# Kernel tuning notes

Measured on AMD Instinct MI355X. Metric: run time of the kernel, lower is better.

The kernel has to match this reference:

```python
import jax, jax.numpy as jnp
import numpy as np

B, S, H = 2, 2048, 1024
NH, HD = 16, 64  # num heads, head dim
EPS = 1e-12


def setup_inputs() -> dict:
    key = jax.random.key(0)
    ks = jax.random.split(key, 10)
    scale = 0.02
    return {
        "hidden_states": jax.random.normal(ks[0], (B, S, H), jnp.float32),
        "attention_mask": jnp.zeros((B, 1, 1, S), jnp.float32),
        "Wq": jax.random.normal(ks[1], (H, H), jnp.float32) * scale,
        "bq": jnp.zeros((H,), jnp.float32),
        "Wk": jax.random.normal(ks[2], (H, H), jnp.float32) * scale,
        "bk": jnp.zeros((H,), jnp.float32),
        "Wv": jax.random.normal(ks[3], (H, H), jnp.float32) * scale,
        "bv": jnp.zeros((H,), jnp.float32),
        "Wo": jax.random.normal(ks[4], (H, H), jnp.float32) * scale,
        "bo": jnp.zeros((H,), jnp.float32),
        "ln_gamma": jnp.ones((H,), jnp.float32),
        "ln_beta": jnp.zeros((H,), jnp.float32),
    }


def _split_heads(x):
    # [B,S,H] -> [B,NH,S,HD]
    b, s, _ = x.shape
    return x.reshape(b, s, NH, HD).transpose(0, 2, 1, 3)


def reference(hidden_states, attention_mask, Wq, bq, Wk, bk, Wv, bv, Wo, bo, ln_gamma, ln_beta):
    q = _split_heads(hidden_states @ Wq + bq)
    k = _split_heads(hidden_states @ Wk + bk)
    v = _split_heads(hidden_states @ Wv + bv)

    # unfused SDPA, as in source: matmul -> scale -> mask -> softmax -> matmul
    scores = jnp.einsum('bhqd,bhkd->bhqk', q, k) / jnp.sqrt(jnp.float32(HD))
    scores = scores + attention_mask
    probs = jax.nn.softmax(scores, axis=-1)  # dropout p=0 (eval)
    ctx = jnp.einsum('bhqk,bhkd->bhqd', probs, v)
    ctx = ctx.transpose(0, 2, 1, 3).reshape(hidden_states.shape)  # [B,S,H]

    # BaseBertSelfOutput: dense -> (dropout p=0) -> LayerNorm(residual)
    out = ctx @ Wo + bo
    res = out + hidden_states
    mu = jnp.mean(res, axis=-1, keepdims=True)
    var = jnp.mean(jnp.square(res - mu), axis=-1, keepdims=True)
    normed = (res - mu) * jax.lax.rsqrt(var + EPS)
    return normed * ln_gamma + ln_beta
```

## Files before the change

kernel.cpp:

```cpp
#include <hip/hip_runtime.h>
#include <hip/hip_bf16.h>

#define B_  2
#define S_  2048
#define H_  1024
#define NH_ 16
#define HD_ 64
#define EPSLN 1e-12f
#define LOG2E 1.4426950408889634f

typedef short bf16x8 __attribute__((ext_vector_type(8)));
typedef float f32x4  __attribute__((ext_vector_type(4)));
typedef float f32x16 __attribute__((ext_vector_type(16)));
typedef unsigned int u32x4 __attribute__((ext_vector_type(4)));

__device__ __forceinline__ float bf2f(ushort u) {
    union { unsigned int i; float f; } v; v.i = ((unsigned int)u) << 16; return v.f;
}
__device__ __forceinline__ ushort f2bf(float f) {
    union { float f; unsigned int i; } v; v.f = f;
    unsigned int r = v.i + 0x7FFFu + ((v.i >> 16) & 1u);
    return (ushort)(r >> 16);
}
__device__ __forceinline__ ushort f2bf_hw(float f) {
    __hip_bfloat16 h = __float2bfloat16(f);
    return *reinterpret_cast<ushort*>(&h);
}
__device__ __forceinline__ unsigned int pack_bf2(float a, float b) {
    return ((unsigned int)f2bf_hw(b) << 16) | (unsigned int)f2bf_hw(a);
}

__device__ __forceinline__ bf16x8 mk_pfrag(float a0, float a1, float a2, float a3,
                                           float a4, float a5, float a6, float a7, int hi) {
    unsigned int Lo0 = pack_bf2(a0, a1);
    unsigned int Lo1 = pack_bf2(a2, a3);
    unsigned int Hi0 = pack_bf2(a4, a5);
    unsigned int Hi1 = pack_bf2(a6, a7);
    unsigned int sLo0 = (unsigned int)__shfl_xor((int)Lo0, 32, 64);
    unsigned int sLo1 = (unsigned int)__shfl_xor((int)Lo1, 32, 64);
    unsigned int sHi0 = (unsigned int)__shfl_xor((int)Hi0, 32, 64);
    unsigned int sHi1 = (unsigned int)__shfl_xor((int)Hi1, 32, 64);
    u32x4 d;
    d.x = hi ? sHi0 : Lo0;
    d.y = hi ? sHi1 : Lo1;
    d.z = hi ? Hi0 : sLo0;
    d.w = hi ? Hi1 : sLo1;
    return __builtin_bit_cast(bf16x8, d);
}

__global__ __launch_bounds__(256) void cvt_f32_bf16(const float* __restrict__ in,
                                                    ushort* __restrict__ out, int n) {
    int i = (blockIdx.x * 256 + threadIdx.x) * 4;
    float4 v = *(const float4*)&in[i];
    ushort4 o = make_ushort4(f2bf(v.x), f2bf(v.y), f2bf(v.z), f2bf(v.w));
    *(ushort4*)&out[i] = o;
}

__global__ __launch_bounds__(256) void scale_mask(const float* __restrict__ in,
                                                  float* __restrict__ out) {
    int i = blockIdx.x * 256 + threadIdx.x;
    out[i] = in[i] * LOG2E;
}

__global__ __launch_bounds__(256) void transpose_cvt(
        const float* __restrict__ W0, const float* __restrict__ W1,
        const float* __restrict__ W2, const float* __restrict__ W3,
        ushort* __restrict__ T0, ushort* __restrict__ T1,
        ushort* __restrict__ T2, ushort* __restrict__ T3) {
    const int z = blockIdx.z;
    const float* in = (z == 0) ? W0 : (z == 1) ? W1 : (z == 2) ? W2 : W3;
    ushort* out     = (z == 0) ? T0 : (z == 1) ? T1 : (z == 2) ? T2 : T3;

    __shared__ float tile[64][65];
    const int bx = blockIdx.x * 64, by = blockIdx.y * 64;
    const int t = threadIdx.x;
    #pragma unroll
    for (int i = 0; i < 16; i++) {
        int idx = t + i * 256;
        int r = idx >> 6, c = idx & 63;
        tile[r][c] = in[(by + r) * 1024 + bx + c];
    }
    __syncthreads();
    #pragma unroll
    for (int i = 0; i < 16; i++) {
        int idx = t + i * 256;
        int r = idx >> 6, c = idx & 63;
        out[(bx + r) * 1024 + by + c] = f2bf(tile[c][r]);
    }
}

__global__ __launch_bounds__(256) void v_transpose(const ushort* __restrict__ Vb,
                                                   ushort* __restrict__ VtG) {
    __shared__ ushort tile[64][72];
    const int s0 = blockIdx.x * 64;
    const int head = blockIdx.y;
    const ushort* src = Vb + (size_t)head * S_ * HD_;
    ushort* dst       = VtG + (size_t)head * S_ * HD_;
    const int t = threadIdx.x, lane = t & 63, w = t >> 6;

    uint4 a = *(const uint4*)&src[(s0 + lane) * HD_ + w * 16];
    uint4 b = *(const uint4*)&src[(s0 + lane) * HD_ + w * 16 + 8];
    const ushort* pa = (const ushort*)&a;
    #pragma unroll
    for (int i = 0; i < 8; i++) tile[w * 16 + i][lane] = pa[i];
    const ushort* pb = (const ushort*)&b;
    #pragma unroll
    for (int i = 0; i < 8; i++) tile[w * 16 + 8 + i][lane] = pb[i];
    __syncthreads();

    const int d = t >> 2, sc = (t & 3) * 16;
    uint4 o1 = *(const uint4*)&tile[d][sc];
    uint4 o2 = *(const uint4*)&tile[d][sc + 8];
    *(uint4*)&dst[d * S_ + s0 + sc]     = o1;
    *(uint4*)&dst[d * S_ + s0 + sc + 8] = o2;
}

__global__ __launch_bounds__(256) void qkv_gemm(
        const ushort* __restrict__ X,
        const ushort* __restrict__ Wqt, const ushort* __restrict__ Wkt, const ushort* __restrict__ Wvt,
        const float* __restrict__ bq,  const float* __restrict__ bk,  const float* __restrict__ bv,
        ushort* __restrict__ Qo, ushort* __restrict__ Ko, ushort* __restrict__ Vo) {
    const int which = blockIdx.z;
    const ushort* Wt  = (which == 0) ? Wqt : (which == 1) ? Wkt : Wvt;
    const float* bias = (which == 0) ? bq  : (which == 1) ? bk  : bv;
    ushort* Out       = (which == 0) ? Qo  : (which == 1) ? Ko  : Vo;

    __shared__ ushort As[128][72];
    __shared__ ushort Bs[128][72];
    const int m0 = blockIdx.x * 128, n0 = blockIdx.y * 128;
    const int t = threadIdx.x;
    const int lane = t & 63, w = t >> 6;
    const int wr = (w >> 1) * 64, wc = (w & 1) * 64;
    const int l15 = lane & 15, l4 = lane >> 4;

    f32x4 acc[4][4] = {};
    const int sr = t >> 3, sc = (t & 7) * 8;

    for (int k0 = 0; k0 < H_; k0 += 64) {
        __syncthreads();
        #pragma unroll
        for (int p = 0; p < 4; p++) {
            uint4 av  = *(const uint4*)&X [(m0 + p * 32 + sr) * H_ + k0 + sc];
            uint4 bv2 = *(const uint4*)&Wt[(n0 + p * 32 + sr) * H_ + k0 + sc];
            *(uint4*)&As[p * 32 + sr][sc] = av;
            *(uint4*)&Bs[p * 32 + sr][sc] = bv2;
        }
        __syncthreads();
        #pragma unroll
        for (int ks = 0; ks < 2; ks++) {
            bf16x8 af[4], bfr[4];
            #pragma unroll
            for (int i = 0; i < 4; i++) af[i]  = *(const bf16x8*)&As[wr + i * 16 + l15][ks * 32 + l4 * 8];
            #pragma unroll
            for (int i = 0; i < 4; i++) bfr[i] = *(const bf16x8*)&Bs[wc + i * 16 + l15][ks * 32 + l4 * 8];
            #pragma unroll
            for (int mi = 0; mi < 4; mi++)
                #pragma unroll
                for (int ni = 0; ni < 4; ni++)
                    acc[mi][ni] = __builtin_amdgcn_mfma_f32_16x16x32_bf16(af[mi], bfr[ni], acc[mi][ni], 0, 0, 0);
        }
    }

    #pragma unroll
    for (int ni = 0; ni < 4; ni++) {
        int n = n0 + wc + ni * 16 + l15;
        float bvf = bias[n];
        int h = n >> 6, d = n & 63;
        #pragma unroll
        for (int mi = 0; mi < 4; mi++) {
            int mrow = m0 + wr + mi * 16 + l4 * 4;
            #pragma unroll
            for (int j = 0; j < 4; j++) {
                int m = mrow + j;
                int b = m >> 11, s = m & 2047;
                Out[((b * NH_ + h) * S_ + s) * HD_ + d] = f2bf(acc[mi][ni][j] + bvf);
            }
        }
    }
}

__global__ __launch_bounds__(128) void flash_attn(
        const ushort* __restrict__ Q, const ushort* __restrict__ K, const ushort* __restrict__ VtG,
        const float* __restrict__ maskL2, ushort* __restrict__ ctx) {
    __shared__ __align__(16) ushort Ks[64][72];
    __shared__ __align__(16) ushort Vt[64][72];

    const int wgid = blockIdx.x;
    const int vid  = (wgid & 7) * 128 + (wgid >> 3);
    const int qt   = vid & 31;
    const int hb   = vid >> 5;
    const int h    = hb & (NH_ - 1), b = hb >> 4;

    const int t = threadIdx.x, lane = t & 63, w = t >> 6;
    const int l31 = lane & 31, hi = lane >> 5;
    const size_t head_off = (size_t)hb * S_ * HD_;
    const ushort* Qh = Q + head_off;
    const ushort* Kh = K + head_off;
    const ushort* Vh = VtG + head_off;

    const int q0w  = qt * 64 + w * 32;
    const int qrow = q0w + l31;
    bf16x8 qf[4];
    #pragma unroll
    for (int kc = 0; kc < 4; kc++)
        qf[kc] = *(const bf16x8*)&Qh[qrow * 64 + kc * 16 + hi * 8];

    f32x16 acc0 = {}, acc1 = {};
    float mrun = -1e30f, lrun = 0.f;

    const float ksc = 0.125f * LOG2E;

    for (int kv0 = 0; kv0 < S_; kv0 += 64) {
        __syncthreads();
        #pragma unroll
        for (int it = 0; it < 4; it++) {
            int ci = it * 128 + t;
            int row = ci >> 3, ce = (ci & 7) * 8;
            *(uint4*)&Ks[row][ce] = *(const uint4*)&Kh[(kv0 + row) * 64 + ce];
            *(uint4*)&Vt[row][ce] = *(const uint4*)&Vh[row * S_ + kv0 + ce];
        }
        __syncthreads();

        f32x16 s0 = {}, s1 = {};
        #pragma unroll
        for (int kc = 0; kc < 4; kc++) {
            bf16x8 kf0 = *(const bf16x8*)&Ks[l31][kc * 16 + hi * 8];
            bf16x8 kf1 = *(const bf16x8*)&Ks[32 + l31][kc * 16 + hi * 8];
            s0 = __builtin_amdgcn_mfma_f32_32x32x16_bf16(kf0, qf[kc], s0, 0, 0, 0);
            s1 = __builtin_amdgcn_mfma_f32_32x32x16_bf16(kf1, qf[kc], s1, 0, 0, 0);
        }

        float tmax = -1e30f;
        #pragma unroll
        for (int g = 0; g < 4; g++) {
            float4 mk0 = *(const float4*)&maskL2[b * S_ + kv0 + g * 8 + hi * 4];
            float4 mk1 = *(const float4*)&maskL2[b * S_ + kv0 + 32 + g * 8 + hi * 4];
            #pragma unroll
            for (int j = 0; j < 4; j++) {
                int r = g * 4 + j;
                s0[r] = fmaf(s0[r], ksc, (&mk0.x)[j]);
                s1[r] = fmaf(s1[r], ksc, (&mk1.x)[j]);
                tmax = fmaxf(tmax, fmaxf(s0[r], s1[r]));
            }
        }
        tmax = fmaxf(tmax, __shfl_xor(tmax, 32, 64));

        if (!__all(tmax <= mrun + 8.0f)) {
            float mnew  = fmaxf(mrun, tmax);
            float scale = exp2f(mrun - mnew);
            mrun = mnew;
            lrun *= scale;
            #pragma unroll
            for (int r = 0; r < 16; r++) { acc0[r] *= scale; acc1[r] *= scale; }
        }

        float tsum = 0.f;
        #pragma unroll
        for (int r = 0; r < 16; r++) {
            s0[r] = exp2f(s0[r] - mrun);
            s1[r] = exp2f(s1[r] - mrun);
            tsum += s0[r] + s1[r];
        }
        tsum += __shfl_xor(tsum, 32, 64);
        lrun += tsum;

        bf16x8 pf0 = mk_pfrag(s0[0], s0[1], s0[2],  s0[3],  s0[4],  s0[5],  s0[6],  s0[7],  hi);
        bf16x8 pf1 = mk_pfrag(s0[8], s0[9], s0[10], s0[11], s0[12], s0[13], s0[14], s0[15], hi);
        bf16x8 pf2 = mk_pfrag(s1[0], s1[1], s1[2],  s1[3],  s1[4],  s1[5],  s1[6],  s1[7],  hi);
        bf16x8 pf3 = mk_pfrag(s1[8], s1[9], s1[10], s1[11], s1[12], s1[13], s1[14], s1[15], hi);

        {
            bf16x8 vf0, vf1;
            vf0 = *(const bf16x8*)&Vt[l31][0 * 16 + hi * 8];
            vf1 = *(const bf16x8*)&Vt[32 + l31][0 * 16 + hi * 8];
            acc0 = __builtin_amdgcn_mfma_f32_32x32x16_bf16(vf0, pf0, acc0, 0, 0, 0);
            acc1 = __builtin_amdgcn_mfma_f32_32x32x16_bf16(vf1, pf0, acc1, 0, 0, 0);
            vf0 = *(const bf16x8*)&Vt[l31][1 * 16 + hi * 8];
            vf1 = *(const bf16x8*)&Vt[32 + l31][1 * 16 + hi * 8];
            acc0 = __builtin_amdgcn_mfma_f32_32x32x16_bf16(vf0, pf1, acc0, 0, 0, 0);
            acc1 = __builtin_amdgcn_mfma_f32_32x32x16_bf16(vf1, pf1, acc1, 0, 0, 0);
            vf0 = *(const bf16x8*)&Vt[l31][2 * 16 + hi * 8];
            vf1 = *(const bf16x8*)&Vt[32 + l31][2 * 16 + hi * 8];
            acc0 = __builtin_amdgcn_mfma_f32_32x32x16_bf16(vf0, pf2, acc0, 0, 0, 0);
            acc1 = __builtin_amdgcn_mfma_f32_32x32x16_bf16(vf1, pf2, acc1, 0, 0, 0);
            vf0 = *(const bf16x8*)&Vt[l31][3 * 16 + hi * 8];
            vf1 = *(const bf16x8*)&Vt[32 + l31][3 * 16 + hi * 8];
            acc0 = __builtin_amdgcn_mfma_f32_32x32x16_bf16(vf0, pf3, acc0, 0, 0, 0);
            acc1 = __builtin_amdgcn_mfma_f32_32x32x16_bf16(vf1, pf3, acc1, 0, 0, 0);
        }
    }

    const float inv = 1.0f / lrun;
    const size_t rowbase = ((size_t)b * S_ + q0w + l31) * H_ + h * 64;
    #pragma unroll
    for (int g = 0; g < 4; g++) {
        ushort4 o0, o1;
        o0.x = f2bf(acc0[g * 4 + 0] * inv); o0.y = f2bf(acc0[g * 4 + 1] * inv);
        o0.z = f2bf(acc0[g * 4 + 2] * inv); o0.w = f2bf(acc0[g * 4 + 3] * inv);
        o1.x = f2bf(acc1[g * 4 + 0] * inv); o1.y = f2bf(acc1[g * 4 + 1] * inv);
        o1.z = f2bf(acc1[g * 4 + 2] * inv); o1.w = f2bf(acc1[g * 4 + 3] * inv);
        *(ushort4*)&ctx[rowbase + g * 8 + hi * 4]      = o0;
        *(ushort4*)&ctx[rowbase + 32 + g * 8 + hi * 4] = o1;
    }
}

__global__ __launch_bounds__(256) void out_proj(
        const ushort* __restrict__ Ctx, const ushort* __restrict__ Wot,
        const float* __restrict__ bo,  const float* __restrict__ Hs,
        float* __restrict__ Tmp) {
    __shared__ ushort As[128][72];
    __shared__ ushort Bs[128][72];
    const int m0 = blockIdx.x * 128, n0 = blockIdx.y * 128;
    const int t = threadIdx.x;
    const int lane = t & 63, w = t >> 6;
    const int wr = (w >> 1) * 64, wc = (w & 1) * 64;
    const int l15 = lane & 15, l4 = lane >> 4;

    f32x4 acc[4][4] = {};
    const int sr = t >> 3, sc = (t & 7) * 8;

    for (int k0 = 0; k0 < H_; k0 += 64) {
        __syncthreads();
        #pragma unroll
        for (int p = 0; p < 4; p++) {
            uint4 av  = *(const uint4*)&Ctx[(m0 + p * 32 + sr) * H_ + k0 + sc];
            uint4 bv2 = *(const uint4*)&Wot[(n0 + p * 32 + sr) * H_ + k0 + sc];
            *(uint4*)&As[p * 32 + sr][sc] = av;
            *(uint4*)&Bs[p * 32 + sr][sc] = bv2;
        }
        __syncthreads();
        #pragma unroll
        for (int ks = 0; ks < 2; ks++) {
            bf16x8 af[4], bfr[4];
            #pragma unroll
            for (int i = 0; i < 4; i++) af[i]  = *(const bf16x8*)&As[wr + i * 16 + l15][ks * 32 + l4 * 8];
            #pragma unroll
            for (int i = 0; i < 4; i++) bfr[i] = *(const bf16x8*)&Bs[wc + i * 16 + l15][ks * 32 + l4 * 8];
            #pragma unroll
            for (int mi = 0; mi < 4; mi++)
                #pragma unroll
                for (int ni = 0; ni < 4; ni++)
                    acc[mi][ni] = __builtin_amdgcn_mfma_f32_16x16x32_bf16(af[mi], bfr[ni], acc[mi][ni], 0, 0, 0);
        }
    }

    #pragma unroll
    for (int ni = 0; ni < 4; ni++) {
        int n = n0 + wc + ni * 16 + l15;
        float bvf = bo[n];
        #pragma unroll
        for (int mi = 0; mi < 4; mi++) {
            int mrow = m0 + wr + mi * 16 + l4 * 4;
            #pragma unroll
            for (int j = 0; j < 4; j++) {
                int m = mrow + j;
                Tmp[(size_t)m * H_ + n] = acc[mi][ni][j] + bvf + Hs[(size_t)m * H_ + n];
            }
        }
    }
}

__global__ __launch_bounds__(256) void ln_kernel(
        const float* __restrict__ Tmp, const float* __restrict__ gamma,
        const float* __restrict__ beta, float* __restrict__ Out) {
    const int row = blockIdx.x;
    const float* x = Tmp + (size_t)row * H_;
    const int t = threadIdx.x, w = t >> 6, lane = t & 63;

    float4 v = *(const float4*)&x[t * 4];
    float s = v.x + v.y + v.z + v.w;
    #pragma unroll
    for (int m = 1; m < 64; m <<= 1) s += __shfl_xor(s, m, 64);
    __shared__ float red[4], red2[4];
    if (lane == 0) red[w] = s;
    __syncthreads();
    float mu = (red[0] + red[1] + red[2] + red[3]) * (1.0f / H_);

    float d0 = v.x - mu, d1 = v.y - mu, d2 = v.z - mu, d3 = v.w - mu;
    float sq = d0 * d0 + d1 * d1 + d2 * d2 + d3 * d3;
    #pragma unroll
    for (int m = 1; m < 64; m <<= 1) sq += __shfl_xor(sq, m, 64);
    if (lane == 0) red2[w] = sq;
    __syncthreads();
    float var = (red2[0] + red2[1] + red2[2] + red2[3]) * (1.0f / H_);
    float rstd = rsqrtf(var + EPSLN);

    float dd[4] = {d0, d1, d2, d3};
    float4 o;
    o.x = dd[0] * rstd * gamma[t * 4 + 0] + beta[t * 4 + 0];
    o.y = dd[1] * rstd * gamma[t * 4 + 1] + beta[t * 4 + 1];
    o.z = dd[2] * rstd * gamma[t * 4 + 2] + beta[t * 4 + 2];
    o.w = dd[3] * rstd * gamma[t * 4 + 3] + beta[t * 4 + 3];
    *(float4*)&Out[(size_t)row * H_ + t * 4] = o;
}

extern "C" void kernel_launch(void* const* d_in, const int* in_sizes, int n_in,
                              void* d_out, int out_size, void* d_ws, size_t ws_size,
                              hipStream_t stream) {
    const float* hs    = (const float*)d_in[0];
    const float* mask  = (const float*)d_in[1];
    const float* Wq    = (const float*)d_in[2];
    const float* bq    = (const float*)d_in[3];
    const float* Wk    = (const float*)d_in[4];
    const float* bk    = (const float*)d_in[5];
    const float* Wv    = (const float*)d_in[6];
    const float* bv    = (const float*)d_in[7];
    const float* Wo    = (const float*)d_in[8];
    const float* bo    = (const float*)d_in[9];
    const float* gamma = (const float*)d_in[10];
    const float* beta  = (const float*)d_in[11];

    char* ws = (char*)d_ws;
    const size_t WSZ = (size_t)H_ * H_;
    const size_t TSZ = (size_t)B_ * S_ * H_;
    ushort* Wqt = (ushort*)ws;
    ushort* Wkt = Wqt + WSZ;
    ushort* Wvt = Wkt + WSZ;
    ushort* Wot = Wvt + WSZ;
    ushort* Xb  = Wot + WSZ;
    ushort* Qb  = Xb + TSZ;
    ushort* Kb  = Qb + TSZ;
    ushort* Vb  = Kb + TSZ;
    ushort* Ctx = Vb + TSZ;
    float*  Tmp = (float*)(Ctx + TSZ);
    ushort* VtG = (ushort*)Tmp;
    float* MaskL2 = (float*)Xb;

    cvt_f32_bf16<<<TSZ / (256 * 4), 256, 0, stream>>>(hs, Xb, (int)TSZ);
    transpose_cvt<<<dim3(16, 16, 4), 256, 0, stream>>>(Wq, Wk, Wv, Wo, Wqt, Wkt, Wvt, Wot);

    qkv_gemm<<<dim3(32, 8, 3), 256, 0, stream>>>(Xb, Wqt, Wkt, Wvt, bq, bk, bv, Qb, Kb, Vb);
    scale_mask<<<(B_ * S_) / 256, 256, 0, stream>>>(mask, MaskL2);
    v_transpose<<<dim3(S_ / 64, B_ * NH_), 256, 0, stream>>>(Vb, VtG);
    flash_attn<<<dim3(1024), 128, 0, stream>>>(Qb, Kb, VtG, MaskL2, Ctx);
    out_proj<<<dim3(32, 8), 256, 0, stream>>>(Ctx, Wot, bo, hs, Tmp);
    ln_kernel<<<B_ * S_, 256, 0, stream>>>(Tmp, gamma, beta, (float*)d_out);
}
```

Baseline: 169.7 us.

## Double-buffer K/V tiles with async global-to-LDS loads and XOR swizzle

```diff
diff --git a/kernel.cpp b/kernel.cpp
--- a/kernel.cpp
+++ b/kernel.cpp
@@ -28,6 +28,11 @@
 }
 __device__ __forceinline__ unsigned int pack_bf2(float a, float b) {
     return ((unsigned int)f2bf_hw(b) << 16) | (unsigned int)f2bf_hw(a);
+}
+
+__device__ __forceinline__ void gll16(const ushort* g, ushort* l) {
+    __builtin_amdgcn_global_load_lds((const __attribute__((address_space(1))) void*)g,
+                                     (__attribute__((address_space(3))) void*)l, 16, 0, 0);
 }
 
 __device__ __forceinline__ bf16x8 mk_pfrag(float a0, float a1, float a2, float a3,
@@ -182,8 +187,8 @@
 __global__ __launch_bounds__(128) void flash_attn(
         const ushort* __restrict__ Q, const ushort* __restrict__ K, const ushort* __restrict__ VtG,
         const float* __restrict__ maskL2, ushort* __restrict__ ctx) {
-    __shared__ __align__(16) ushort Ks[64][72];
-    __shared__ __align__(16) ushort Vt[64][72];
+    __shared__ __align__(16) ushort KsB[2][4096];
+    __shared__ __align__(16) ushort VtB[2][4096];
 
     const int wgid = blockIdx.x;
     const int vid  = (wgid & 7) * 128 + (wgid >> 3);
@@ -207,25 +212,40 @@
 
     f32x16 acc0 = {}, acc1 = {};
     float mrun = -1e30f, lrun = 0.f;
-
     const float ksc = 0.125f * LOG2E;
-
+    const int xm = (l31 & 7) << 3;
+
+    #pragma unroll
+    for (int it = 0; it < 4; it++) {
+        int ci = it * 128 + t;
+        int row = ci >> 3;
+        int ce = ((ci & 7) * 8) ^ ((row & 7) << 3);
+        gll16(&Kh[row * 64 + ce],  &KsB[0][it * 1024 + w * 512]);
+        gll16(&Vh[row * S_ + ce],  &VtB[0][it * 1024 + w * 512]);
+    }
+
+    int cur = 0;
     for (int kv0 = 0; kv0 < S_; kv0 += 64) {
         __syncthreads();
-        #pragma unroll
-        for (int it = 0; it < 4; it++) {
-            int ci = it * 128 + t;
-            int row = ci >> 3, ce = (ci & 7) * 8;
-            *(uint4*)&Ks[row][ce] = *(const uint4*)&Kh[(kv0 + row) * 64 + ce];
-            *(uint4*)&Vt[row][ce] = *(const uint4*)&Vh[row * S_ + kv0 + ce];
-        }
-        __syncthreads();
+        if (kv0 + 64 < S_) {
+            #pragma unroll
+            for (int it = 0; it < 4; it++) {
+                int ci = it * 128 + t;
+                int row = ci >> 3;
+                int ce = ((ci & 7) * 8) ^ ((row & 7) << 3);
+                gll16(&Kh[(kv0 + 64 + row) * 64 + ce], &KsB[cur ^ 1][it * 1024 + w * 512]);
+                gll16(&Vh[row * S_ + kv0 + 64 + ce],   &VtB[cur ^ 1][it * 1024 + w * 512]);
+            }
+        }
+        const ushort* KsL = KsB[cur];
+        const ushort* VtL = VtB[cur];
 
         f32x16 s0 = {}, s1 = {};
         #pragma unroll
         for (int kc = 0; kc < 4; kc++) {
-            bf16x8 kf0 = *(const bf16x8*)&Ks[l31][kc * 16 + hi * 8];
-            bf16x8 kf1 = *(const bf16x8*)&Ks[32 + l31][kc * 16 + hi * 8];
+            int ec = kc * 16 + hi * 8;
+            bf16x8 kf0 = *(const bf16x8*)&KsL[l31 * 64 + (ec ^ xm)];
+            bf16x8 kf1 = *(const bf16x8*)&KsL[(32 + l31) * 64 + (ec ^ xm)];
             s0 = __builtin_amdgcn_mfma_f32_32x32x16_bf16(kf0, qf[kc], s0, 0, 0, 0);
             s1 = __builtin_amdgcn_mfma_f32_32x32x16_bf16(kf1, qf[kc], s1, 0, 0, 0);
         }
@@ -271,23 +291,24 @@
 
         {
             bf16x8 vf0, vf1;
-            vf0 = *(const bf16x8*)&Vt[l31][0 * 16 + hi * 8];
-            vf1 = *(const bf16x8*)&Vt[32 + l31][0 * 16 + hi * 8];
+            vf0 = *(const bf16x8*)&VtL[l31 * 64 + ((0 * 16 + hi * 8) ^ xm)];
+            vf1 = *(const bf16x8*)&VtL[(32 + l31) * 64 + ((0 * 16 + hi * 8) ^ xm)];
             acc0 = __builtin_amdgcn_mfma_f32_32x32x16_bf16(vf0, pf0, acc0, 0, 0, 0);
             acc1 = __builtin_amdgcn_mfma_f32_32x32x16_bf16(vf1, pf0, acc1, 0, 0, 0);
-            vf0 = *(const bf16x8*)&Vt[l31][1 * 16 + hi * 8];
-            vf1 = *(const bf16x8*)&Vt[32 + l31][1 * 16 + hi * 8];
+            vf0 = *(const bf16x8*)&VtL[l31 * 64 + ((1 * 16 + hi * 8) ^ xm)];
+            vf1 = *(const bf16x8*)&VtL[(32 + l31) * 64 + ((1 * 16 + hi * 8) ^ xm)];
             acc0 = __builtin_amdgcn_mfma_f32_32x32x16_bf16(vf0, pf1, acc0, 0, 0, 0);
             acc1 = __builtin_amdgcn_mfma_f32_32x32x16_bf16(vf1, pf1, acc1, 0, 0, 0);
-            vf0 = *(const bf16x8*)&Vt[l31][2 * 16 + hi * 8];
-            vf1 = *(const bf16x8*)&Vt[32 + l31][2 * 16 + hi * 8];
+            vf0 = *(const bf16x8*)&VtL[l31 * 64 + ((2 * 16 + hi * 8) ^ xm)];
+            vf1 = *(const bf16x8*)&VtL[(32 + l31) * 64 + ((2 * 16 + hi * 8) ^ xm)];
             acc0 = __builtin_amdgcn_mfma_f32_32x32x16_bf16(vf0, pf2, acc0, 0, 0, 0);
             acc1 = __builtin_amdgcn_mfma_f32_32x32x16_bf16(vf1, pf2, acc1, 0, 0, 0);
-            vf0 = *(const bf16x8*)&Vt[l31][3 * 16 + hi * 8];
-            vf1 = *(const bf16x8*)&Vt[32 + l31][3 * 16 + hi * 8];
+            vf0 = *(const bf16x8*)&VtL[l31 * 64 + ((3 * 16 + hi * 8) ^ xm)];
+            vf1 = *(const bf16x8*)&VtL[(32 + l31) * 64 + ((3 * 16 + hi * 8) ^ xm)];
             acc0 = __builtin_amdgcn_mfma_f32_32x32x16_bf16(vf0, pf3, acc0, 0, 0, 0);
             acc1 = __builtin_amdgcn_mfma_f32_32x32x16_bf16(vf1, pf3, acc1, 0, 0, 0);
         }
+        cur ^= 1;
     }
 
     const float inv = 1.0f / lrun;
```

After: 175.5 us. +3.4%, slower.

## Split attention KV range in two and merge partials in a combine kernel

Applied to the files above, without the earlier changes.

```diff
diff --git a/kernel.cpp b/kernel.cpp
--- a/kernel.cpp
+++ b/kernel.cpp
@@ -181,15 +181,17 @@
 
 __global__ __launch_bounds__(128) void flash_attn(
         const ushort* __restrict__ Q, const ushort* __restrict__ K, const ushort* __restrict__ VtG,
-        const float* __restrict__ maskL2, ushort* __restrict__ ctx) {
+        const float* __restrict__ maskL2, ushort* __restrict__ Part, float2* __restrict__ ML) {
     __shared__ __align__(16) ushort Ks[64][72];
     __shared__ __align__(16) ushort Vt[64][72];
 
     const int wgid = blockIdx.x;
-    const int vid  = (wgid & 7) * 128 + (wgid >> 3);
-    const int qt   = vid & 31;
-    const int hb   = vid >> 5;
-    const int h    = hb & (NH_ - 1), b = hb >> 4;
+    const int vid  = (wgid & 7) * 256 + (wgid >> 3);
+    const int split = vid & 1;
+    const int qt    = (vid >> 1) & 31;
+    const int hb    = vid >> 6;
+    const int b     = hb >> 4;
+    const int kbase = split << 10;
 
     const int t = threadIdx.x, lane = t & 63, w = t >> 6;
     const int l31 = lane & 31, hi = lane >> 5;
@@ -207,10 +209,9 @@
 
     f32x16 acc0 = {}, acc1 = {};
     float mrun = -1e30f, lrun = 0.f;
-
     const float ksc = 0.125f * LOG2E;
 
-    for (int kv0 = 0; kv0 < S_; kv0 += 64) {
+    for (int kv0 = kbase; kv0 < kbase + 1024; kv0 += 64) {
         __syncthreads();
         #pragma unroll
         for (int it = 0; it < 4; it++) {
@@ -290,18 +291,48 @@
         }
     }
 
-    const float inv = 1.0f / lrun;
+    ushort* Pp = Part + (size_t)split * (B_ * S_ * H_);
+    const int h = hb & (NH_ - 1);
     const size_t rowbase = ((size_t)b * S_ + q0w + l31) * H_ + h * 64;
     #pragma unroll
     for (int g = 0; g < 4; g++) {
         ushort4 o0, o1;
-        o0.x = f2bf(acc0[g * 4 + 0] * inv); o0.y = f2bf(acc0[g * 4 + 1] * inv);
-        o0.z = f2bf(acc0[g * 4 + 2] * inv); o0.w = f2bf(acc0[g * 4 + 3] * inv);
-        o1.x = f2bf(acc1[g * 4 + 0] * inv); o1.y = f2bf(acc1[g * 4 + 1] * inv);
-        o1.z = f2bf(acc1[g * 4 + 2] * inv); o1.w = f2bf(acc1[g * 4 + 3] * inv);
-        *(ushort4*)&ctx[rowbase + g * 8 + hi * 4]      = o0;
-        *(ushort4*)&ctx[rowbase + 32 + g * 8 + hi * 4] = o1;
-    }
+        o0.x = f2bf(acc0[g * 4 + 0]); o0.y = f2bf(acc0[g * 4 + 1]);
+        o0.z = f2bf(acc0[g * 4 + 2]); o0.w = f2bf(acc0[g * 4 + 3]);
+        o1.x = f2bf(acc1[g * 4 + 0]); o1.y = f2bf(acc1[g * 4 + 1]);
+        o1.z = f2bf(acc1[g * 4 + 2]); o1.w = f2bf(acc1[g * 4 + 3]);
+        *(ushort4*)&Pp[rowbase + g * 8 + hi * 4]      = o0;
+        *(ushort4*)&Pp[rowbase + 32 + g * 8 + hi * 4] = o1;
+    }
+    if (hi == 0)
+        ML[(size_t)split * (B_ * NH_ * S_) + (size_t)hb * S_ + q0w + l31] = make_float2(mrun, lrun);
+}
+
+__global__ __launch_bounds__(256) void combine_kv(
+        const ushort* __restrict__ P0, const ushort* __restrict__ P1,
+        const float2* __restrict__ ML0, const float2* __restrict__ ML1,
+        ushort* __restrict__ ctx) {
+    const int row = blockIdx.x;
+    const int t = threadIdx.x;
+    const int b = row >> 11, s = row & 2047;
+    const int col = t * 4;
+    const int h = col >> 6;
+    const int hb = b * NH_ + h;
+
+    float2 a = ML0[(size_t)hb * S_ + s];
+    float2 c = ML1[(size_t)hb * S_ + s];
+    float M  = fmaxf(a.x, c.x);
+    float e0 = exp2f(a.x - M), e1 = exp2f(c.x - M);
+    float inv = 1.0f / (a.y * e0 + c.y * e1);
+
+    ushort4 p0 = *(const ushort4*)&P0[(size_t)row * H_ + col];
+    ushort4 p1 = *(const ushort4*)&P1[(size_t)row * H_ + col];
+    ushort4 o;
+    o.x = f2bf((bf2f(p0.x) * e0 + bf2f(p1.x) * e1) * inv);
+    o.y = f2bf((bf2f(p0.y) * e0 + bf2f(p1.y) * e1) * inv);
+    o.z = f2bf((bf2f(p0.z) * e0 + bf2f(p1.z) * e1) * inv);
+    o.w = f2bf((bf2f(p0.w) * e0 + bf2f(p1.w) * e1) * inv);
+    *(ushort4*)&ctx[(size_t)row * H_ + col] = o;
 }
 
 __global__ __launch_bounds__(256) void out_proj(
@@ -423,8 +454,10 @@
     ushort* Vb  = Kb + TSZ;
     ushort* Ctx = Vb + TSZ;
     float*  Tmp = (float*)(Ctx + TSZ);
-    ushort* VtG = (ushort*)Tmp;
-    float* MaskL2 = (float*)Xb;
+    float*  MaskL2 = (float*)Wqt;
+    float2* ML     = (float2*)Wkt;
+    ushort* VtG    = Xb;
+    ushort* Part   = (ushort*)Tmp;
 
     cvt_f32_bf16<<<TSZ / (256 * 4), 256, 0, stream>>>(hs, Xb, (int)TSZ);
     transpose_cvt<<<dim3(16, 16, 4), 256, 0, stream>>>(Wq, Wk, Wv, Wo, Wqt, Wkt, Wvt, Wot);
@@ -432,7 +465,9 @@
     qkv_gemm<<<dim3(32, 8, 3), 256, 0, stream>>>(Xb, Wqt, Wkt, Wvt, bq, bk, bv, Qb, Kb, Vb);
     scale_mask<<<(B_ * S_) / 256, 256, 0, stream>>>(mask, MaskL2);
     v_transpose<<<dim3(S_ / 64, B_ * NH_), 256, 0, stream>>>(Vb, VtG);
-    flash_attn<<<dim3(1024), 128, 0, stream>>>(Qb, Kb, VtG, MaskL2, Ctx);
+    flash_attn<<<dim3(2048), 128, 0, stream>>>(Qb, Kb, VtG, MaskL2, Part, ML);
+    combine_kv<<<dim3(B_ * S_), 256, 0, stream>>>(Part, Part + TSZ,
+                                                  ML, ML + (size_t)B_ * NH_ * S_, Ctx);
     out_proj<<<dim3(32, 8), 256, 0, stream>>>(Ctx, Wot, bo, hs, Tmp);
     ln_kernel<<<B_ * S_, 256, 0, stream>>>(Tmp, gamma, beta, (float*)d_out);
 }
```

Result: slower. 200.3 us (+18.1%).

## Use direct global-to-LDS loads in GEMMs and widen flash-attention workgroups

Applied to the files above, without the earlier changes.

```diff
diff --git a/kernel.cpp b/kernel.cpp
--- a/kernel.cpp
+++ b/kernel.cpp
@@ -28,6 +28,11 @@
 }
 __device__ __forceinline__ unsigned int pack_bf2(float a, float b) {
     return ((unsigned int)f2bf_hw(b) << 16) | (unsigned int)f2bf_hw(a);
+}
+
+__device__ __forceinline__ void gll16(const ushort* g, ushort* l) {
+    __builtin_amdgcn_global_load_lds((const __attribute__((address_space(1))) void*)g,
+                                     (__attribute__((address_space(3))) void*)l, 16, 0, 0);
 }
 
 __device__ __forceinline__ bf16x8 mk_pfrag(float a0, float a1, float a2, float a3,
@@ -125,8 +130,8 @@
     const float* bias = (which == 0) ? bq  : (which == 1) ? bk  : bv;
     ushort* Out       = (which == 0) ? Qo  : (which == 1) ? Ko  : Vo;
 
-    __shared__ ushort As[128][72];
-    __shared__ ushort Bs[128][72];
+    __shared__ __align__(16) ushort As[128 * 64];
+    __shared__ __align__(16) ushort Bs[128 * 64];
     const int m0 = blockIdx.x * 128, n0 = blockIdx.y * 128;
     const int t = threadIdx.x;
     const int lane = t & 63, w = t >> 6;
@@ -134,31 +139,30 @@
     const int l15 = lane & 15, l4 = lane >> 4;
 
     f32x4 acc[4][4] = {};
-    const int sr = t >> 3, sc = (t & 7) * 8;
 
     for (int k0 = 0; k0 < H_; k0 += 64) {
-        __syncthreads();
-        #pragma unroll
-        for (int p = 0; p < 4; p++) {
-            uint4 av  = *(const uint4*)&X [(m0 + p * 32 + sr) * H_ + k0 + sc];
-            uint4 bv2 = *(const uint4*)&Wt[(n0 + p * 32 + sr) * H_ + k0 + sc];
-            *(uint4*)&As[p * 32 + sr][sc] = av;
-            *(uint4*)&Bs[p * 32 + sr][sc] = bv2;
+        #pragma unroll
+        for (int it = 0; it < 4; it++) {
+            int ci = it * 256 + t;
+            int row = ci >> 3, col = (ci & 7) * 8;
+            gll16(&X [(m0 + row) * H_ + k0 + col], &As[ci * 8]);
+            gll16(&Wt[(n0 + row) * H_ + k0 + col], &Bs[ci * 8]);
         }
         __syncthreads();
         #pragma unroll
         for (int ks = 0; ks < 2; ks++) {
             bf16x8 af[4], bfr[4];
             #pragma unroll
-            for (int i = 0; i < 4; i++) af[i]  = *(const bf16x8*)&As[wr + i * 16 + l15][ks * 32 + l4 * 8];
-            #pragma unroll
-            for (int i = 0; i < 4; i++) bfr[i] = *(const bf16x8*)&Bs[wc + i * 16 + l15][ks * 32 + l4 * 8];
+            for (int i = 0; i < 4; i++) af[i]  = *(const bf16x8*)&As[(wr + i * 16 + l15) * 64 + ks * 32 + l4 * 8];
+            #pragma unroll
+            for (int i = 0; i < 4; i++) bfr[i] = *(const bf16x8*)&Bs[(wc + i * 16 + l15) * 64 + ks * 32 + l4 * 8];
             #pragma unroll
             for (int mi = 0; mi < 4; mi++)
                 #pragma unroll
                 for (int ni = 0; ni < 4; ni++)
                     acc[mi][ni] = __builtin_amdgcn_mfma_f32_16x16x32_bf16(af[mi], bfr[ni], acc[mi][ni], 0, 0, 0);
         }
+        __syncthreads();
     }
 
     #pragma unroll
@@ -179,16 +183,16 @@
     }
 }
 
-__global__ __launch_bounds__(128) void flash_attn(
+__global__ __launch_bounds__(256) void flash_attn(
         const ushort* __restrict__ Q, const ushort* __restrict__ K, const ushort* __restrict__ VtG,
         const float* __restrict__ maskL2, ushort* __restrict__ ctx) {
     __shared__ __align__(16) ushort Ks[64][72];
     __shared__ __align__(16) ushort Vt[64][72];
 
     const int wgid = blockIdx.x;
-    const int vid  = (wgid & 7) * 128 + (wgid >> 3);
-    const int qt   = vid & 31;
-    const int hb   = vid >> 5;
+    const int vid  = (wgid & 7) * 64 + (wgid >> 3);
+    const int qt   = vid & 15;
+    const int hb   = vid >> 4;
     const int h    = hb & (NH_ - 1), b = hb >> 4;
 
     const int t = threadIdx.x, lane = t & 63, w = t >> 6;
@@ -198,7 +202,7 @@
     const ushort* Kh = K + head_off;
     const ushort* Vh = VtG + head_off;
 
-    const int q0w  = qt * 64 + w * 32;
+    const int q0w  = qt * 128 + w * 32;
     const int qrow = q0w + l31;
     bf16x8 qf[4];
     #pragma unroll
@@ -207,14 +211,13 @@
 
     f32x16 acc0 = {}, acc1 = {};
     float mrun = -1e30f, lrun = 0.f;
-
     const float ksc = 0.125f * LOG2E;
 
     for (int kv0 = 0; kv0 < S_; kv0 += 64) {
         __syncthreads();
         #pragma unroll
-        for (int it = 0; it < 4; it++) {
-            int ci = it * 128 + t;
+        for (int it = 0; it < 2; it++) {
+            int ci = it * 256 + t;
             int row = ci >> 3, ce = (ci & 7) * 8;
             *(uint4*)&Ks[row][ce] = *(const uint4*)&Kh[(kv0 + row) * 64 + ce];
             *(uint4*)&Vt[row][ce] = *(const uint4*)&Vh[row * S_ + kv0 + ce];
@@ -308,8 +311,8 @@
         const ushort* __restrict__ Ctx, const ushort* __restrict__ Wot,
         const float* __restrict__ bo,  const float* __restrict__ Hs,
         float* __restrict__ Tmp) {
-    __shared__ ushort As[128][72];
-    __shared__ ushort Bs[128][72];
+    __shared__ __align__(16) ushort As[128 * 64];
+    __shared__ __align__(16) ushort Bs[128 * 64];
     const int m0 = blockIdx.x * 128, n0 = blockIdx.y * 128;
     const int t = threadIdx.x;
     const int lane = t & 63, w = t >> 6;
@@ -317,31 +320,30 @@
     const int l15 = lane & 15, l4 = lane >> 4;
 
     f32x4 acc[4][4] = {};
-    const int sr = t >> 3, sc = (t & 7) * 8;
 
     for (int k0 = 0; k0 < H_; k0 += 64) {
-        __syncthreads();
-        #pragma unroll
-        for (int p = 0; p < 4; p++) {
-            uint4 av  = *(const uint4*)&Ctx[(m0 + p * 32 + sr) * H_ + k0 + sc];
-            uint4 bv2 = *(const uint4*)&Wot[(n0 + p * 32 + sr) * H_ + k0 + sc];
-            *(uint4*)&As[p * 32 + sr][sc] = av;
-            *(uint4*)&Bs[p * 32 + sr][sc] = bv2;
+        #pragma unroll
+        for (int it = 0; it < 4; it++) {
+            int ci = it * 256 + t;
+            int row = ci >> 3, col = (ci & 7) * 8;
+            gll16(&Ctx[(m0 + row) * H_ + k0 + col], &As[ci * 8]);
+            gll16(&Wot[(n0 + row) * H_ + k0 + col], &Bs[ci * 8]);
         }
         __syncthreads();
         #pragma unroll
         for (int ks = 0; ks < 2; ks++) {
             bf16x8 af[4], bfr[4];
             #pragma unroll
-            for (int i = 0; i < 4; i++) af[i]  = *(const bf16x8*)&As[wr + i * 16 + l15][ks * 32 + l4 * 8];
-            #pragma unroll
-            for (int i = 0; i < 4; i++) bfr[i] = *(const bf16x8*)&Bs[wc + i * 16 + l15][ks * 32 + l4 * 8];
+            for (int i = 0; i < 4; i++) af[i]  = *(const bf16x8*)&As[(wr + i * 16 + l15) * 64 + ks * 32 + l4 * 8];
+            #pragma unroll
+            for (int i = 0; i < 4; i++) bfr[i] = *(const bf16x8*)&Bs[(wc + i * 16 + l15) * 64 + ks * 32 + l4 * 8];
             #pragma unroll
             for (int mi = 0; mi < 4; mi++)
                 #pragma unroll
                 for (int ni = 0; ni < 4; ni++)
                     acc[mi][ni] = __builtin_amdgcn_mfma_f32_16x16x32_bf16(af[mi], bfr[ni], acc[mi][ni], 0, 0, 0);
         }
+        __syncthreads();
     }
 
     #pragma unroll
@@ -432,7 +434,7 @@
     qkv_gemm<<<dim3(32, 8, 3), 256, 0, stream>>>(Xb, Wqt, Wkt, Wvt, bq, bk, bv, Qb, Kb, Vb);
     scale_mask<<<(B_ * S_) / 256, 256, 0, stream>>>(mask, MaskL2);
     v_transpose<<<dim3(S_ / 64, B_ * NH_), 256, 0, stream>>>(Vb, VtG);
-    flash_attn<<<dim3(1024), 128, 0, stream>>>(Qb, Kb, VtG, MaskL2, Ctx);
+    flash_attn<<<dim3(512), 256, 0, stream>>>(Qb, Kb, VtG, MaskL2, Ctx);
     out_proj<<<dim3(32, 8), 256, 0, stream>>>(Ctx, Wot, bo, hs, Tmp);
     ln_kernel<<<B_ * S_, 256, 0, stream>>>(Tmp, gamma, beta, (float*)d_out);
 }
```

Result: no change. 169.2 us (-0.3%).
